# Kernel tuning notes

Measured on AMD Instinct MI355X. Metric: run time of the kernel, lower is better.

Reference implementation:

```python
import jax, jax.numpy as jnp
import numpy as np

B_, L_, H_ = 2, 2048, 2048          # batch, seq_len, hidden_size
I_, N_, NH, P_ = 4096, 128, 64, 64   # intermediate, ssm_state, num_heads, head_dim
K_, CH = 4, 256                      # conv kernel, chunk size
DT_MIN, DT_MAX = 0.0, 1e10


def setup_inputs() -> dict:
    key = jax.random.key(0)
    ks = jax.random.split(key, 8)
    conv_dim = I_ + 2 * N_
    proj_out = 2 * (I_ + N_) + NH
    return {
        "hidden_states": jax.random.normal(ks[0], (B_, L_, H_), jnp.float32),
        "W_in": jax.random.normal(ks[1], (proj_out, H_), jnp.float32) * 0.02,
        "conv_w": jax.random.normal(ks[2], (conv_dim, 1, K_), jnp.float32) * 0.2,
        "conv_b": jnp.zeros((conv_dim,), jnp.float32),
        "dt_bias": jax.random.uniform(ks[3], (NH,), jnp.float32),
        "A_log": jnp.log(jax.random.uniform(ks[4], (NH,), jnp.float32, 1.0, 16.0)),
        "D": jnp.ones((NH,), jnp.float32),
        "norm_w": jnp.ones((I_,), jnp.float32),
        "W_out": jax.random.normal(ks[5], (H_, I_), jnp.float32) * 0.02,
    }


def _segsum(x):
    # stable segment-sum: out[..., i, j] = sum_{k=j+1..i} x[..., k] for i>=j, else -inf
    T = x.shape[-1]
    xr = jnp.broadcast_to(x[..., None], x.shape + (T,))
    lower = jnp.tril(jnp.ones((T, T), bool), -1)
    s = jnp.cumsum(jnp.where(lower, xr, 0.0), axis=-2)
    return jnp.where(jnp.tril(jnp.ones((T, T), bool)), s, -jnp.inf)


def reference(hidden_states, W_in, conv_w, conv_b, dt_bias, A_log, D, norm_w, W_out):
    b, L, _ = hidden_states.shape
    proj = hidden_states @ W_in.T                       # (b, L, 2*(I+N)+H)
    z, xBC, dt = jnp.split(proj, [I_, 2 * I_ + 2 * N_], axis=-1)

    # depthwise causal conv1d + silu
    x_t = xBC.transpose(0, 2, 1)                        # (b, conv_dim, L)
    conv = jax.lax.conv_general_dilated(
        x_t, conv_w, (1,), [(K_ - 1, 0)],
        dimension_numbers=("NCH", "OIH", "NCH"), feature_group_count=I_ + 2 * N_)
    xBC = jax.nn.silu((conv + conv_b[None, :, None]).transpose(0, 2, 1))
    x, Bm, Cm = jnp.split(xBC, [I_, I_ + N_], axis=-1)  # (b,L,I) (b,L,N) (b,L,N)

    # ---- SSD naive (chunked state-space-duality scan) ----
    A = -jnp.exp(A_log.astype(jnp.float32))             # (h,)
    dt = jnp.clip(jax.nn.softplus(dt + dt_bias), DT_MIN, DT_MAX)  # (b,L,h)
    x4 = x.reshape(b, L, NH, P_)
    pad = (-L) % CH
    padf = lambda t: jnp.pad(t, [(0, 0), (0, pad)] + [(0, 0)] * (t.ndim - 2))
    D_res = D[None, None, :, None] * padf(x4)           # (b, Lp, h, p)
    xs = padf(x4 * dt[..., None])
    Ah = padf(A[None, None, :] * dt)                    # (b, Lp, h)
    Bc, Cc = padf(Bm), padf(Cm)
    c = (L + pad) // CH
    xs = xs.reshape(b, c, CH, NH, P_)                   # (b,c,l,h,p)
    Ah = Ah.reshape(b, c, CH, NH).transpose(0, 3, 1, 2) # (b,h,c,l)
    Bc = Bc.reshape(b, c, CH, N_)
    Cc = Cc.reshape(b, c, CH, N_)

    A_cs = jnp.cumsum(Ah, axis=-1)                      # (b,h,c,l)
    Lm = jnp.exp(_segsum(Ah))                           # (b,h,c,l,l)
    # intra-chunk (diagonal block) output; B/C shared across heads (n_groups=1)
    Y_diag = jnp.einsum("bcln,bcsn,bhcls,bcshp->bclhp", Cc, Bc, Lm, xs)

    decay_states = jnp.exp(A_cs[..., -1:] - A_cs)       # (b,h,c,l)
    states = jnp.einsum("bcln,bhcl,bclhp->bchpn", Bc, decay_states, xs)
    states = jnp.concatenate([jnp.zeros_like(states[:, :1]), states], axis=1)
    decay_chunk = jnp.exp(_segsum(jnp.pad(A_cs[..., -1], [(0, 0), (0, 0), (1, 0)])))
    new_states = jnp.einsum("bhzc,bchpn->bzhpn", decay_chunk, states)
    states = new_states[:, :-1]                         # (b,c,h,p,n)
    Y_off = jnp.einsum("bcln,bchpn,bhcl->bclhp", Cc, states, jnp.exp(A_cs))

    y = (Y_diag + Y_off).reshape(b, c * CH, NH, P_) + D_res
    y = y[:, :L].reshape(b, L, I_)

    # gated RMSNorm (normalize=True: multiply by silu(residual) before norm)
    yf = y.astype(jnp.float32) * jax.nn.silu(z.astype(jnp.float32))
    yf = yf * jax.lax.rsqrt(jnp.mean(yf * yf, -1, keepdims=True) + 1e-5) * norm_w
    return yf.astype(hidden_states.dtype) @ W_out.T
```

## Files before the change

kernel.cpp:

```cpp
#include <hip/hip_runtime.h>
#include <hip/hip_bf16.h>
#include <math.h>


#define B_SZ 2
#define L_SZ 2048
#define H_SZ 2048
#define I_SZ 4096
#define N_SZ 128
#define NH_SZ 64
#define P_SZ 64
#define CH_SZ 256
#define NC_SZ 8
#define PROJ_SZ 8512
#define CONV_SZ 4352
#define XOFF 4096
#define DTOFF 8448
#define BOFF 4096
#define COFF 4224

typedef __attribute__((ext_vector_type(8))) short short8_t;
typedef __attribute__((ext_vector_type(4))) float float4_t;

#define GLDS(gp, lp)                                                   \
  __builtin_amdgcn_global_load_lds(                                    \
      (const __attribute__((address_space(1))) void*)(gp),             \
      (__attribute__((address_space(3))) void*)(lp), 16, 0, 0)

__device__ __forceinline__ float bf2f(unsigned short u) {
  union { unsigned int i; float f; } v; v.i = ((unsigned int)u) << 16; return v.f;
}
__device__ __forceinline__ unsigned short f2bf(float f) {
  union { float f; unsigned int i; } v; v.f = f;
  unsigned int b = v.i + 0x7fffu + ((v.i >> 16) & 1u);
  return (unsigned short)(b >> 16);
}
__device__ __forceinline__ void unpack8(uint4 v, float* f) {
  f[0] = bf2f((unsigned short)(v.x & 0xffffu)); f[1] = bf2f((unsigned short)(v.x >> 16));
  f[2] = bf2f((unsigned short)(v.y & 0xffffu)); f[3] = bf2f((unsigned short)(v.y >> 16));
  f[4] = bf2f((unsigned short)(v.z & 0xffffu)); f[5] = bf2f((unsigned short)(v.z >> 16));
  f[6] = bf2f((unsigned short)(v.w & 0xffffu)); f[7] = bf2f((unsigned short)(v.w >> 16));
}
__device__ __forceinline__ float silu_f(float x) { return x / (1.f + expf(-x)); }

__device__ __forceinline__ float load1(const void* p, long long e, int fp32) {
  return fp32 ? ((const float*)p)[e] : bf2f(((const unsigned short*)p)[e]);
}
__device__ __forceinline__ void load4(const void* p, long long e, int fp32, float* f) {
  if (fp32) {
    float4 a = *(const float4*)((const float*)p + e);
    f[0] = a.x; f[1] = a.y; f[2] = a.z; f[3] = a.w;
  } else {
    uint2 v = *(const uint2*)((const unsigned short*)p + e);
    f[0] = bf2f((unsigned short)(v.x & 0xffffu)); f[1] = bf2f((unsigned short)(v.x >> 16));
    f[2] = bf2f((unsigned short)(v.y & 0xffffu)); f[3] = bf2f((unsigned short)(v.y >> 16));
  }
}
__device__ __forceinline__ void load8(const void* p, long long e, int fp32, float* f) {
  if (fp32) {
    float4 a = *(const float4*)((const float*)p + e);
    float4 b = *(const float4*)((const float*)p + e + 4);
    f[0] = a.x; f[1] = a.y; f[2] = a.z; f[3] = a.w;
    f[4] = b.x; f[5] = b.y; f[6] = b.z; f[7] = b.w;
  } else {
    uint4 v = *(const uint4*)((const unsigned short*)p + e);
    unpack8(v, f);
  }
}

__global__ void detect_k(const void* p0, const void* p1, const void* p2,
                         const void* p3, const void* p4, const void* p5,
                         const void* p6, const void* p7, const void* p8,
                         int n0, int n1, int n2, int n3, int n4, int n5,
                         int n6, int n7, int n8, int* flags) {
  __shared__ int pe, po;
  const void* ps[9] = {p0, p1, p2, p3, p4, p5, p6, p7, p8};
  int ns[9] = {n0, n1, n2, n3, n4, n5, n6, n7, n8};
  int t = threadIdx.x;
  for (int i = 0; i < 9; i++) {
    if (t == 0) { pe = 0; po = 0; }
    __syncthreads();
    int S = ns[i] < 256 ? ns[i] : 256;
    if (t < S) {
      unsigned short u = ((const unsigned short*)ps[i])[t];
      int ex = (u >> 7) & 0xFF;
      int plaus = ((u & 0x7FFFu) != 0) && (ex >= 0x70) && (ex <= 0x8F);
      if (plaus) { if (t & 1) atomicAdd(&po, 1); else atomicAdd(&pe, 1); }
    }
    __syncthreads();
    if (t == 0) flags[i] = (2 * pe < po) ? 1 : 0;
    __syncthreads();
  }
  if (t == 0) { flags[14] = 0; flags[15] = 0; }
}

__global__ __launch_bounds__(256)
void cvt_bf16_k(const void* __restrict__ src, unsigned short* __restrict__ dst,
                long long n8, const int* __restrict__ flags, int fi) {
  long long g = (long long)blockIdx.x * 256 + threadIdx.x;
  if (g >= n8) return;
  long long e = g * 8;
  if (flags[fi]) {
    const float* s = (const float*)src + e;
    float4 a = *(const float4*)s;
    float4 b = *(const float4*)(s + 4);
    unsigned short o[8] = {f2bf(a.x), f2bf(a.y), f2bf(a.z), f2bf(a.w),
                           f2bf(b.x), f2bf(b.y), f2bf(b.z), f2bf(b.w)};
    *(uint4*)(dst + e) = *(const uint4*)o;
  } else {
    *(uint4*)(dst + e) = *(const uint4*)((const unsigned short*)src + e);
  }
}

template <int OUT_MODE>
__global__ __launch_bounds__(256)
void gemm_dma_k(const unsigned short* __restrict__ A,
                const unsigned short* __restrict__ B,
                void* __restrict__ Cptr, int M, int N, int K,
                int lda, int ldb, int ldc,
                const int* __restrict__ flags, int fo) {
  __shared__ unsigned short As[128 * 32];
  __shared__ unsigned short Bs[128 * 32];
  const int t = threadIdx.x;
  const int lane = t & 63;
  const int wave = t >> 6;
  const int quad = lane >> 4;
  const int l16 = lane & 15;
  const int m0 = blockIdx.y * 128, n0 = blockIdx.x * 128;
  const int wm = (wave >> 1) * 64, wn = (wave & 1) * 64;
  const int ofp = (OUT_MODE == 2) ? flags[fo] : 0;

  float4_t acc[4][4];
#pragma unroll
  for (int i = 0; i < 4; i++)
#pragma unroll
    for (int j = 0; j < 4; j++) acc[i][j] = (float4_t){0.f, 0.f, 0.f, 0.f};

  const int rr = lane >> 2;
  const int ks = (lane & 3) * 8;
  const long long aR0 = (long long)(m0 + wave * 16 + rr) * lda + ks;
  const long long aR1 = aR0 + (long long)64 * lda;
  const long long bR0 = (long long)(n0 + wave * 16 + rr) * ldb + ks;
  const long long bR1 = bR0 + (long long)64 * ldb;
  unsigned short* asd0 = &As[(wave * 16) * 32];
  unsigned short* asd1 = &As[(64 + wave * 16) * 32];
  unsigned short* bsd0 = &Bs[(wave * 16) * 32];
  unsigned short* bsd1 = &Bs[(64 + wave * 16) * 32];

  for (int k0 = 0; k0 < K; k0 += 32) {
    __syncthreads();
    GLDS(A + aR0 + k0, asd0);
    GLDS(A + aR1 + k0, asd1);
    GLDS(B + bR0 + k0, bsd0);
    GLDS(B + bR1 + k0, bsd1);
    __syncthreads();
    short8_t afr[4], bfr[4];
#pragma unroll
    for (int i = 0; i < 4; i++)
      afr[i] = *(const short8_t*)&As[(wm + i * 16 + l16) * 32 + quad * 8];
#pragma unroll
    for (int j = 0; j < 4; j++)
      bfr[j] = *(const short8_t*)&Bs[(wn + j * 16 + l16) * 32 + quad * 8];
#pragma unroll
    for (int i = 0; i < 4; i++)
#pragma unroll
      for (int j = 0; j < 4; j++)
        acc[i][j] = __builtin_amdgcn_mfma_f32_16x16x32_bf16(
            afr[i], bfr[j], acc[i][j], 0, 0, 0);
  }
#pragma unroll
  for (int i = 0; i < 4; i++) {
#pragma unroll
    for (int r = 0; r < 4; r++) {
      const int m = m0 + wm + i * 16 + quad * 4 + r;
      const long long base = (long long)m * ldc;
#pragma unroll
      for (int j = 0; j < 4; j++) {
        const int n = n0 + wn + j * 16 + l16;
        if (n < N) {
          float v = acc[i][j][r];
          if (ofp) ((float*)Cptr)[base + n] = v;
          else     ((unsigned short*)Cptr)[base + n] = f2bf(v);
        }
      }
    }
  }
}

template <int OUT_MODE>
__global__ __launch_bounds__(256)
void gemm_bt_k(const void* __restrict__ A, const void* __restrict__ B,
               void* __restrict__ Cptr, int M, int N, int K,
               int lda, int ldb, int ldc,
               long long sA, long long sB, long long sC,
               const int* __restrict__ flags, int fa, int fb, int fo) {
  __shared__ float As[128][20];
  __shared__ float Bs[128][20];
  const int t = threadIdx.x;
  const int tx = t & 15, ty = t >> 4;
  const int m0 = blockIdx.y * 128, n0 = blockIdx.x * 128;
  const int afp = flags[fa], bfp = flags[fb];
  const int ofp = (OUT_MODE == 2) ? flags[fo] : (OUT_MODE == 1);
  const long long zoff = (long long)blockIdx.z;
  float* Cf = (float*)Cptr + zoff * sC;
  unsigned short* Cb = (unsigned short*)Cptr + zoff * sC;

  float acc[8][8];
#pragma unroll
  for (int i = 0; i < 8; i++)
#pragma unroll
    for (int j = 0; j < 8; j++) acc[i][j] = 0.f;

  const int rowS = t >> 1;
  const int kof  = (t & 1) * 8;
  const long long aRow = zoff * sA + (long long)(m0 + rowS) * lda + kof;
  const long long bRow = zoff * sB + (long long)(n0 + rowS) * ldb + kof;
  const bool bOK = (n0 + rowS) < N;

  for (int k0 = 0; k0 < K; k0 += 16) {
    float af[8], bf[8];
    load8(A, aRow + k0, afp, af);
    if (bOK) load8(B, bRow + k0, bfp, bf);
    else { bf[0]=bf[1]=bf[2]=bf[3]=bf[4]=bf[5]=bf[6]=bf[7]=0.f; }
    __syncthreads();
    *(float4*)&As[rowS][kof]     = make_float4(af[0], af[1], af[2], af[3]);
    *(float4*)&As[rowS][kof + 4] = make_float4(af[4], af[5], af[6], af[7]);
    *(float4*)&Bs[rowS][kof]     = make_float4(bf[0], bf[1], bf[2], bf[3]);
    *(float4*)&Bs[rowS][kof + 4] = make_float4(bf[4], bf[5], bf[6], bf[7]);
    __syncthreads();
#pragma unroll
    for (int kk = 0; kk < 16; kk += 2) {
      float2 a2[8], b2[8];
#pragma unroll
      for (int i = 0; i < 8; i++) a2[i] = *(const float2*)&As[ty + 16 * i][kk];
#pragma unroll
      for (int j = 0; j < 8; j++) b2[j] = *(const float2*)&Bs[tx + 16 * j][kk];
#pragma unroll
      for (int i = 0; i < 8; i++)
#pragma unroll
        for (int j = 0; j < 8; j++) {
          acc[i][j] = fmaf(a2[i].x, b2[j].x, acc[i][j]);
          acc[i][j] = fmaf(a2[i].y, b2[j].y, acc[i][j]);
        }
    }
  }
#pragma unroll
  for (int i = 0; i < 8; i++) {
    const int m = m0 + ty + 16 * i;
    const long long base = (long long)m * ldc;
#pragma unroll
    for (int j = 0; j < 8; j++) {
      const int n = n0 + tx + 16 * j;
      if (n < N) {
        if (ofp) Cf[base + n] = acc[i][j];
        else     Cb[base + n] = f2bf(acc[i][j]);
      }
    }
  }
}

__global__ __launch_bounds__(256)
void conv_silu_k(const unsigned short* __restrict__ proj,
                 const void* __restrict__ cw,
                 const void* __restrict__ cb,
                 unsigned short* __restrict__ convx,
                 const int* __restrict__ flags) {
  const int total = B_SZ * L_SZ * (CONV_SZ / 4);
  int g = blockIdx.x * 256 + threadIdx.x;
  if (g >= total) return;
  const int fw = flags[2], fb = flags[3];
  int c4 = g % (CONV_SZ / 4);
  int bl = g / (CONV_SZ / 4);
  int l = bl & (L_SZ - 1);
  int ch = c4 * 4;
  float w0[8], w1[8];
  load8(cw, (long long)ch * 4, fw, w0);
  load8(cw, (long long)ch * 4 + 8, fw, w1);
  float accv[4];
  load4(cb, ch, fb, accv);
  float acc0 = accv[0], acc1 = accv[1], acc2 = accv[2], acc3 = accv[3];
  const long long rb = (long long)(bl - l);
#pragma unroll
  for (int k = 0; k < 4; k++) {
    int ls = l - 3 + k;
    if (ls < 0) continue;
    uint2 xv = *(const uint2*)(proj + (rb + ls) * PROJ_SZ + XOFF + ch);
    float x0 = bf2f((unsigned short)(xv.x & 0xffffu));
    float x1 = bf2f((unsigned short)(xv.x >> 16));
    float x2 = bf2f((unsigned short)(xv.y & 0xffffu));
    float x3 = bf2f((unsigned short)(xv.y >> 16));
    acc0 = fmaf(x0, w0[k], acc0);
    acc1 = fmaf(x1, w0[4 + k], acc1);
    acc2 = fmaf(x2, w1[k], acc2);
    acc3 = fmaf(x3, w1[4 + k], acc3);
  }
  unsigned short o0 = f2bf(silu_f(acc0));
  unsigned short o1 = f2bf(silu_f(acc1));
  unsigned short o2 = f2bf(silu_f(acc2));
  unsigned short o3 = f2bf(silu_f(acc3));
  *(uint2*)(convx + (long long)bl * CONV_SZ + ch) =
      make_uint2((unsigned int)o0 | ((unsigned int)o1 << 16),
                 (unsigned int)o2 | ((unsigned int)o3 << 16));
}

__global__ __launch_bounds__(256)
void dt_prep_k(const unsigned short* __restrict__ proj,
               const void* __restrict__ dt_bias,
               float* __restrict__ dtv, const int* __restrict__ flags) {
  int g = blockIdx.x * 256 + threadIdx.x;
  int h = g & 63;
  long long bl = g >> 6;
  float v = bf2f(proj[bl * PROJ_SZ + DTOFF + h]) + load1(dt_bias, h, flags[4]);
  float sp = (v > 20.f) ? v : log1pf(expf(v));
  dtv[g] = sp;
}

__global__ __launch_bounds__(256)
void acs_scan_k(const float* __restrict__ dtv,
                const void* __restrict__ A_log,
                float* __restrict__ acs, const int* __restrict__ flags) {
  __shared__ float sd[256];
  int blk = blockIdx.x;
  int h = blk & 63;
  int bc = blk >> 6;
  int l = threadIdx.x;
  float Ah = -expf(load1(A_log, h, flags[5]));
  long long row = (long long)bc * CH_SZ + l;
  sd[l] = Ah * dtv[row * NH_SZ + h];
  for (int off = 1; off < 256; off <<= 1) {
    __syncthreads();
    float tv = (l >= off) ? sd[l - off] : 0.f;
    __syncthreads();
    sd[l] += tv;
  }
  acs[(long long)blk * CH_SZ + l] = sd[l];
}

__global__ __launch_bounds__(256)
void chunk_states_k(const unsigned short* __restrict__ convx,
                    const float* __restrict__ dtv,
                    const float* __restrict__ acs,
                    float* __restrict__ stc) {
  __shared__ float Bw[32][128];
  __shared__ float xw[32][64];
  int blk = blockIdx.x;
  int h = blk & 63;
  int bc = blk >> 6;
  int t = threadIdx.x;
  const int p0 = (t & 15) * 4, n0 = (t >> 4) * 8;
  const float* acsb = acs + (long long)blk * 256;
  const float alast = acsb[255];
  float acc[4][8];
#pragma unroll
  for (int i = 0; i < 4; i++)
#pragma unroll
    for (int j = 0; j < 8; j++) acc[i][j] = 0.f;
  const long long row0 = (long long)bc * 256;

  for (int lt0 = 0; lt0 < 256; lt0 += 32) {
    __syncthreads();
#pragma unroll
    for (int q = 0; q < 4; q++) {
      int idx4 = (t + 256 * q) * 4;
      int r = idx4 >> 7, n = idx4 & 127;
      uint2 v = *(const uint2*)(convx + (row0 + lt0 + r) * CONV_SZ + BOFF + n);
      Bw[r][n]     = bf2f((unsigned short)(v.x & 0xffffu));
      Bw[r][n + 1] = bf2f((unsigned short)(v.x >> 16));
      Bw[r][n + 2] = bf2f((unsigned short)(v.y & 0xffffu));
      Bw[r][n + 3] = bf2f((unsigned short)(v.y >> 16));
    }
#pragma unroll
    for (int q = 0; q < 2; q++) {
      int idx4 = (t + 256 * q) * 4;
      int r = idx4 >> 6, p = idx4 & 63;
      long long lg = row0 + lt0 + r;
      float sc = dtv[lg * NH_SZ + h] * expf(alast - acsb[lt0 + r]);
      uint2 v = *(const uint2*)(convx + lg * CONV_SZ + h * 64 + p);
      xw[r][p]     = bf2f((unsigned short)(v.x & 0xffffu)) * sc;
      xw[r][p + 1] = bf2f((unsigned short)(v.x >> 16)) * sc;
      xw[r][p + 2] = bf2f((unsigned short)(v.y & 0xffffu)) * sc;
      xw[r][p + 3] = bf2f((unsigned short)(v.y >> 16)) * sc;
    }
    __syncthreads();
#pragma unroll 4
    for (int lt = 0; lt < 32; lt++) {
      float4 xv = *(const float4*)&xw[lt][p0];
      float4 b0 = *(const float4*)&Bw[lt][n0];
      float4 b1 = *(const float4*)&Bw[lt][n0 + 4];
      float xa[4] = {xv.x, xv.y, xv.z, xv.w};
      float ba[8] = {b0.x, b0.y, b0.z, b0.w, b1.x, b1.y, b1.z, b1.w};
#pragma unroll
      for (int i = 0; i < 4; i++)
#pragma unroll
        for (int j = 0; j < 8; j++) acc[i][j] = fmaf(xa[i], ba[j], acc[i][j]);
    }
  }
  float* outb = stc + (long long)blk * 8192;
#pragma unroll
  for (int i = 0; i < 4; i++) {
    *(float4*)&outb[(p0 + i) * 128 + n0] =
        make_float4(acc[i][0], acc[i][1], acc[i][2], acc[i][3]);
    *(float4*)&outb[(p0 + i) * 128 + n0 + 4] =
        make_float4(acc[i][4], acc[i][5], acc[i][6], acc[i][7]);
  }
}

__global__ __launch_bounds__(256)
void recur_k(float* __restrict__ stc, const float* __restrict__ acs) {
  int blk = blockIdx.x;
  int b = blk >> 6, h = blk & 63;
  int t = threadIdx.x;
  float S[32];
#pragma unroll
  for (int j = 0; j < 32; j++) S[j] = 0.f;
  for (int z = 0; z < 8; z++) {
    long long bz = ((long long)b * 8 + z) * 64 + h;
    long long base = bz * 8192;
    float e = expf(acs[bz * 256 + 255]);
#pragma unroll
    for (int j = 0; j < 32; j++) {
      int idx = j * 256 + t;
      float cs = stc[base + idx];
      stc[base + idx] = S[j];
      S[j] = fmaf(e, S[j], cs);
    }
  }
}

__global__ __launch_bounds__(256)
void yoff_k(const unsigned short* __restrict__ convx,
            const float* __restrict__ sti,
            const float* __restrict__ acs,
            const void* __restrict__ Dw,
            float* __restrict__ y, const int* __restrict__ flags) {
  __shared__ float SIt[128][68];
  __shared__ unsigned short Ct[64][128];
  int blk = blockIdx.x;
  int h = blk & 63;
  int bc = blk >> 6;
  int t = threadIdx.x;
  const int txp = t & 15, lq = t >> 4;
  const float Dh = load1(Dw, h, flags[6]);
  const float* sib = sti + (long long)blk * 8192;
#pragma unroll 4
  for (int q = 0; q < 32; q++) {
    int idx = t + 256 * q;
    SIt[idx & 127][idx >> 7] = sib[idx];
  }
  const float* acsb = acs + (long long)blk * 256;
  const long long row0 = (long long)bc * 256;
  for (int ltile = 0; ltile < 4; ltile++) {
    __syncthreads();
#pragma unroll 4
    for (int q = 0; q < 32; q++) {
      int idx = t + 256 * q;
      int lr = idx >> 7, n = idx & 127;
      Ct[lr][n] = convx[(row0 + ltile * 64 + lr) * CONV_SZ + COFF + n];
    }
    __syncthreads();
    float acc[4][4] = {};
#pragma unroll 4
    for (int n = 0; n < 128; n++) {
      float4 sv = *(const float4*)&SIt[n][txp * 4];
      float c0 = bf2f(Ct[lq * 4 + 0][n]);
      float c1 = bf2f(Ct[lq * 4 + 1][n]);
      float c2 = bf2f(Ct[lq * 4 + 2][n]);
      float c3 = bf2f(Ct[lq * 4 + 3][n]);
      acc[0][0] = fmaf(c0, sv.x, acc[0][0]); acc[0][1] = fmaf(c0, sv.y, acc[0][1]);
      acc[0][2] = fmaf(c0, sv.z, acc[0][2]); acc[0][3] = fmaf(c0, sv.w, acc[0][3]);
      acc[1][0] = fmaf(c1, sv.x, acc[1][0]); acc[1][1] = fmaf(c1, sv.y, acc[1][1]);
      acc[1][2] = fmaf(c1, sv.z, acc[1][2]); acc[1][3] = fmaf(c1, sv.w, acc[1][3]);
      acc[2][0] = fmaf(c2, sv.x, acc[2][0]); acc[2][1] = fmaf(c2, sv.y, acc[2][1]);
      acc[2][2] = fmaf(c2, sv.z, acc[2][2]); acc[2][3] = fmaf(c2, sv.w, acc[2][3]);
      acc[3][0] = fmaf(c3, sv.x, acc[3][0]); acc[3][1] = fmaf(c3, sv.y, acc[3][1]);
      acc[3][2] = fmaf(c3, sv.z, acc[3][2]); acc[3][3] = fmaf(c3, sv.w, acc[3][3]);
    }
#pragma unroll
    for (int i = 0; i < 4; i++) {
      int lloc = ltile * 64 + lq * 4 + i;
      long long row = row0 + lloc;
      float ex = expf(acsb[lloc]);
      uint2 xv = *(const uint2*)(convx + row * CONV_SZ + h * 64 + txp * 4);
      float4 o;
      o.x = fmaf(ex, acc[i][0], Dh * bf2f((unsigned short)(xv.x & 0xffffu)));
      o.y = fmaf(ex, acc[i][1], Dh * bf2f((unsigned short)(xv.x >> 16)));
      o.z = fmaf(ex, acc[i][2], Dh * bf2f((unsigned short)(xv.y & 0xffffu)));
      o.w = fmaf(ex, acc[i][3], Dh * bf2f((unsigned short)(xv.y >> 16)));
      *(float4*)&y[row * I_SZ + h * 64 + txp * 4] = o;
    }
  }
}

__global__ __launch_bounds__(256)
void ydiag_k(const unsigned short* __restrict__ convx,
             const float* __restrict__ dtv,
             const float* __restrict__ acs,
             const float* __restrict__ Gmat,
             float* __restrict__ y) {
  __shared__ float acs_s[256];
  __shared__ float xsT[64][68];
  __shared__ float Mt[64][66];
  int blk = blockIdx.x;
  int h = blk & 63;
  int bc = blk >> 6;
  int t = threadIdx.x;
  const int txp = t & 15, lq = t >> 4;
  acs_s[t] = acs[(long long)blk * 256 + t];
  const long long row0 = (long long)bc * 256;
  const float* Gb = Gmat + (long long)bc * 65536;
  for (int ltile = 0; ltile < 4; ltile++) {
    float acc[4][4] = {};
    for (int stile = 0; stile <= ltile; stile++) {
      __syncthreads();
#pragma unroll 4
      for (int q = 0; q < 16; q++) {
        int idx = t + 256 * q;
        int ss = idx >> 6, p = idx & 63;
        long long row = row0 + stile * 64 + ss;
        xsT[ss][p] = bf2f(convx[row * CONV_SZ + h * 64 + p]) * dtv[row * NH_SZ + h];
      }
#pragma unroll 4
      for (int q = 0; q < 16; q++) {
        int idx = t + 256 * q;
        int lr = idx >> 6, ss = idx & 63;
        int lg = ltile * 64 + lr, sg = stile * 64 + ss;
        float m = 0.f;
        if (sg <= lg) m = Gb[(long long)lg * 256 + sg] * expf(acs_s[lg] - acs_s[sg]);
        Mt[lr][ss] = m;
      }
      __syncthreads();
#pragma unroll 4
      for (int ss = 0; ss < 64; ss++) {
        float4 xv = *(const float4*)&xsT[ss][txp * 4];
        float m0 = Mt[lq * 4 + 0][ss];
        float m1 = Mt[lq * 4 + 1][ss];
        float m2 = Mt[lq * 4 + 2][ss];
        float m3 = Mt[lq * 4 + 3][ss];
        acc[0][0] = fmaf(m0, xv.x, acc[0][0]); acc[0][1] = fmaf(m0, xv.y, acc[0][1]);
        acc[0][2] = fmaf(m0, xv.z, acc[0][2]); acc[0][3] = fmaf(m0, xv.w, acc[0][3]);
        acc[1][0] = fmaf(m1, xv.x, acc[1][0]); acc[1][1] = fmaf(m1, xv.y, acc[1][1]);
        acc[1][2] = fmaf(m1, xv.z, acc[1][2]); acc[1][3] = fmaf(m1, xv.w, acc[1][3]);
        acc[2][0] = fmaf(m2, xv.x, acc[2][0]); acc[2][1] = fmaf(m2, xv.y, acc[2][1]);
        acc[2][2] = fmaf(m2, xv.z, acc[2][2]); acc[2][3] = fmaf(m2, xv.w, acc[2][3]);
        acc[3][0] = fmaf(m3, xv.x, acc[3][0]); acc[3][1] = fmaf(m3, xv.y, acc[3][1]);
        acc[3][2] = fmaf(m3, xv.z, acc[3][2]); acc[3][3] = fmaf(m3, xv.w, acc[3][3]);
      }
    }
#pragma unroll
    for (int i = 0; i < 4; i++) {
      long long row = row0 + ltile * 64 + lq * 4 + i;
      float* yp = &y[row * I_SZ + h * 64 + txp * 4];
      float4 cur = *(float4*)yp;
      cur.x += acc[i][0]; cur.y += acc[i][1]; cur.z += acc[i][2]; cur.w += acc[i][3];
      *(float4*)yp = cur;
    }
  }
}

__global__ __launch_bounds__(256)
void norm_k(const float* __restrict__ y,
            const unsigned short* __restrict__ proj,
            const void* __restrict__ nw,
            unsigned short* __restrict__ yfb, const int* __restrict__ flags) {
  __shared__ float red[4];
  __shared__ float sc_s;
  int row = blockIdx.x;
  int t = threadIdx.x;
  const int fn = flags[7];
  const float* yr = y + (long long)row * I_SZ;
  const unsigned short* zr = proj + (long long)row * PROJ_SZ;
  float g[16];
  float ss = 0.f;
#pragma unroll
  for (int q = 0; q < 4; q++) {
    int i0 = q * 1024 + t * 4;
    float4 yv = *(const float4*)&yr[i0];
    uint2 zv = *(const uint2*)&zr[i0];
    float z0 = bf2f((unsigned short)(zv.x & 0xffffu));
    float z1 = bf2f((unsigned short)(zv.x >> 16));
    float z2 = bf2f((unsigned short)(zv.y & 0xffffu));
    float z3 = bf2f((unsigned short)(zv.y >> 16));
    float g0 = yv.x * silu_f(z0), g1 = yv.y * silu_f(z1);
    float g2 = yv.z * silu_f(z2), g3 = yv.w * silu_f(z3);
    g[q * 4 + 0] = g0; g[q * 4 + 1] = g1; g[q * 4 + 2] = g2; g[q * 4 + 3] = g3;
    ss += g0 * g0 + g1 * g1 + g2 * g2 + g3 * g3;
  }
#pragma unroll
  for (int off = 32; off > 0; off >>= 1) ss += __shfl_down(ss, off, 64);
  if ((t & 63) == 0) red[t >> 6] = ss;
  __syncthreads();
  if (t == 0) sc_s = rsqrtf((red[0] + red[1] + red[2] + red[3]) * (1.f / 4096.f) + 1e-5f);
  __syncthreads();
  float sc = sc_s;
#pragma unroll
  for (int q = 0; q < 4; q++) {
    int i0 = q * 1024 + t * 4;
    float nv[4];
    load4(nw, i0, fn, nv);
    unsigned short o0 = f2bf(g[q * 4 + 0] * sc * nv[0]);
    unsigned short o1 = f2bf(g[q * 4 + 1] * sc * nv[1]);
    unsigned short o2 = f2bf(g[q * 4 + 2] * sc * nv[2]);
    unsigned short o3 = f2bf(g[q * 4 + 3] * sc * nv[3]);
    *(uint2*)&yfb[(long long)row * I_SZ + i0] =
        make_uint2((unsigned int)o0 | ((unsigned int)o1 << 16),
                   (unsigned int)o2 | ((unsigned int)o3 << 16));
  }
}

extern "C" void kernel_launch(void* const* d_in, const int* in_sizes, int n_in,
                              void* d_out, int out_size, void* d_ws, size_t ws_size,
                              hipStream_t stream) {
  const void* hs     = d_in[0];
  const void* W_in   = d_in[1];
  const void* conv_w = d_in[2];
  const void* conv_b = d_in[3];
  const void* dt_b   = d_in[4];
  const void* A_log  = d_in[5];
  const void* Dw     = d_in[6];
  const void* nw     = d_in[7];
  const void* W_out  = d_in[8];

  char* ws = (char*)d_ws;
  size_t off = 0;
  auto alloc = [&](size_t bytes) -> void* {
    void* p = ws + off;
    off += (bytes + 255) & ~(size_t)255;
    return p;
  };
  const long long ML = (long long)B_SZ * L_SZ;
  int* flags = (int*)alloc(64);
  unsigned short* proj  = (unsigned short*)alloc(ML * PROJ_SZ * 2);
  unsigned short* convx = (unsigned short*)alloc(ML * CONV_SZ * 2);
  float* dtv  = (float*)alloc(ML * NH_SZ * 4);
  float* acsb = (float*)alloc((long long)B_SZ * NC_SZ * NH_SZ * CH_SZ * 4);
  float* Gm   = (float*)alloc((long long)B_SZ * NC_SZ * CH_SZ * CH_SZ * 4);
  float* stc  = (float*)alloc((long long)B_SZ * NC_SZ * NH_SZ * P_SZ * N_SZ * 4);
  float* yb   = (float*)alloc(ML * I_SZ * 4);
  unsigned short* yfb = (unsigned short*)stc;
  unsigned short* hs_bf   = (unsigned short*)yb;
  unsigned short* Win_bf  = (unsigned short*)yb + 8388608;
  unsigned short* Wout_bf = (unsigned short*)yb;
  (void)n_in; (void)out_size;
  if (off > ws_size) return;

  dim3 blk(256);
  detect_k<<<1, blk, 0, stream>>>(hs, W_in, conv_w, conv_b, dt_b, A_log, Dw, nw, W_out,
                                  in_sizes[0], in_sizes[1], in_sizes[2], in_sizes[3],
                                  in_sizes[4], in_sizes[5], in_sizes[6], in_sizes[7],
                                  in_sizes[8], flags);
  cvt_bf16_k<<<dim3(4096), blk, 0, stream>>>(hs, hs_bf, 1048576LL, flags, 0);
  cvt_bf16_k<<<dim3(8512), blk, 0, stream>>>(W_in, Win_bf, 2179072LL, flags, 1);
  gemm_dma_k<0><<<dim3(67, 32, 1), blk, 0, stream>>>(
      hs_bf, Win_bf, proj, 4096, PROJ_SZ, H_SZ, H_SZ, H_SZ, PROJ_SZ, flags, 15);
  conv_silu_k<<<dim3((B_SZ * L_SZ * (CONV_SZ / 4) + 255) / 256), blk, 0, stream>>>(
      proj, conv_w, conv_b, convx, flags);
  dt_prep_k<<<dim3((unsigned)(ML * NH_SZ / 256)), blk, 0, stream>>>(proj, dt_b, dtv, flags);
  acs_scan_k<<<dim3(B_SZ * NC_SZ * NH_SZ), blk, 0, stream>>>(dtv, A_log, acsb, flags);
  gemm_bt_k<1><<<dim3(2, 2, 16), blk, 0, stream>>>(
      (const unsigned short*)convx + COFF, (const unsigned short*)convx + BOFF,
      Gm, 256, 256, 128, CONV_SZ, CONV_SZ, 256,
      (long long)256 * CONV_SZ, (long long)256 * CONV_SZ, 65536,
      flags, 15, 15, 15);
  chunk_states_k<<<dim3(1024), blk, 0, stream>>>(convx, dtv, acsb, stc);
  recur_k<<<dim3(B_SZ * NH_SZ), blk, 0, stream>>>(stc, acsb);
  yoff_k<<<dim3(1024), blk, 0, stream>>>(convx, stc, acsb, Dw, yb, flags);
  ydiag_k<<<dim3(1024), blk, 0, stream>>>(convx, dtv, acsb, Gm, yb);
  norm_k<<<dim3((unsigned)ML), blk, 0, stream>>>(yb, proj, nw, yfb, flags);
  cvt_bf16_k<<<dim3(4096), blk, 0, stream>>>(W_out, Wout_bf, 1048576LL, flags, 8);
  gemm_dma_k<2><<<dim3(16, 32, 1), blk, 0, stream>>>(
      yfb, Wout_bf, d_out, 4096, H_SZ, I_SZ, I_SZ, I_SZ, H_SZ, flags, 0);
}
```

Baseline: 823.5 us.

## Add 256x256 eight-phase pipelined GEMM for input projection with tile swizzle

```diff
diff --git a/kernel.cpp b/kernel.cpp
--- a/kernel.cpp
+++ b/kernel.cpp
@@ -112,6 +112,163 @@
   }
 }
 
+#define MFMA_ACC(d, a, b) \
+  d = __builtin_amdgcn_mfma_f32_16x16x32_bf16(a, b, d, 0, 0, 0)
+#define LDA_FR(buf, i, kk) \
+  (*(const short8_t*)&As[(buf)*16384 + (wm*128 + (i)*16 + l16)*64 + \
+                         (((((kk)<<2) + quad) ^ l7) << 3)])
+#define LDB_FR(buf, j, kk) \
+  (*(const short8_t*)&Bs[(buf)*16384 + (wn*64 + (j)*16 + l16)*64 + \
+                         (((((kk)<<2) + quad) ^ l7) << 3)])
+#define STAGE_A(h, tile, buf) do {                                          \
+    GLDS(aSrc[h][0] + ((long long)(tile) << 6),                             \
+         &As[(buf)*16384 + (h)*8192 + (wave*16)*64]);                       \
+    GLDS(aSrc[h][1] + ((long long)(tile) << 6),                             \
+         &As[(buf)*16384 + (h)*8192 + (wave*16 + 8)*64]);                   \
+  } while (0)
+#define STAGE_B(h, tile, buf) do {                                          \
+    GLDS(bSrc[h][0] + ((long long)(tile) << 6),                             \
+         &Bs[(buf)*16384 + (h)*8192 + (wave*16)*64]);                       \
+    GLDS(bSrc[h][1] + ((long long)(tile) << 6),                             \
+         &Bs[(buf)*16384 + (h)*8192 + (wave*16 + 8)*64]);                   \
+  } while (0)
+
+__global__ __launch_bounds__(512, 2)
+void gemm_8ph_k(const unsigned short* __restrict__ A,
+                const unsigned short* __restrict__ B,
+                unsigned short* __restrict__ C,
+                int N, int K, int lda, int ldb, int ldc, int gxTiles) {
+  __shared__ alignas(16) unsigned short As[2 * 256 * 64];
+  __shared__ alignas(16) unsigned short Bs[2 * 256 * 64];
+  const int t = threadIdx.x;
+  const int lane = t & 63;
+  const int wave = t >> 6;
+  const int quad = lane >> 4;
+  const int l16 = lane & 15;
+  const int l7 = lane & 7;
+  const int l3 = lane >> 3;
+  const int wm = wave >> 2;
+  const int wn = wave & 3;
+
+  int id = blockIdx.x;
+  const int nwg = gridDim.x;
+  int swz = id;
+  if ((nwg & 7) == 0) swz = (id & 7) * (nwg >> 3) + (id >> 3);
+  const int band = gxTiles << 2;
+  const int by = (swz & 3) + ((swz / band) << 2);
+  const int bx = (swz >> 2) % gxTiles;
+  const int m0 = by << 8;
+  const int n0 = bx << 8;
+  const int NT = K >> 6;
+
+  const int kperm = ((l7 ^ l3) << 3);
+  const unsigned short* aSrc[2][2];
+  const unsigned short* bSrc[2][2];
+#pragma unroll
+  for (int h = 0; h < 2; ++h)
+#pragma unroll
+    for (int c = 0; c < 2; ++c) {
+      const int rloc = h * 128 + wave * 16 + c * 8 + l3;
+      aSrc[h][c] = A + (long long)(m0 + rloc) * lda + kperm;
+      int bn = n0 + rloc;
+      if (bn > N - 1) bn = N - 1;
+      bSrc[h][c] = B + (long long)bn * ldb + kperm;
+    }
+
+  float4_t acc[8][4];
+#pragma unroll
+  for (int i = 0; i < 8; ++i)
+#pragma unroll
+    for (int j = 0; j < 4; ++j) acc[i][j] = (float4_t){0.f, 0.f, 0.f, 0.f};
+
+  STAGE_A(0, 0, 0); STAGE_A(1, 0, 0);
+  STAGE_B(0, 0, 0); STAGE_B(1, 0, 0);
+  STAGE_B(0, 1, 1); STAGE_B(1, 1, 1);
+  asm volatile("s_waitcnt vmcnt(4)" ::: "memory");
+  __builtin_amdgcn_s_barrier();
+
+  short8_t af[4][2], bf[4][2];
+  for (int tt = 0; tt < NT; ++tt) {
+    const int rb = tt & 1, nb = rb ^ 1;
+#pragma unroll
+    for (int i = 0; i < 4; ++i) { af[i][0] = LDA_FR(rb, i, 0); af[i][1] = LDA_FR(rb, i, 1); }
+#pragma unroll
+    for (int j = 0; j < 2; ++j) { bf[j][0] = LDB_FR(rb, j, 0); bf[j][1] = LDB_FR(rb, j, 1); }
+    if (tt + 1 < NT) STAGE_A(0, tt + 1, nb);
+    asm volatile("s_waitcnt lgkmcnt(8)" ::: "memory");
+    __builtin_amdgcn_s_barrier();
+    asm volatile("s_waitcnt lgkmcnt(0)" ::: "memory");
+    __builtin_amdgcn_s_setprio(1);
+#pragma unroll
+    for (int i = 0; i < 4; ++i)
+#pragma unroll
+      for (int j = 0; j < 2; ++j) {
+        MFMA_ACC(acc[i][j], af[i][0], bf[j][0]);
+        MFMA_ACC(acc[i][j], af[i][1], bf[j][1]);
+      }
+    __builtin_amdgcn_s_setprio(0);
+    __builtin_amdgcn_s_barrier();
+#pragma unroll
+    for (int j = 2; j < 4; ++j) { bf[j][0] = LDB_FR(rb, j, 0); bf[j][1] = LDB_FR(rb, j, 1); }
+    if (tt + 1 < NT) STAGE_A(1, tt + 1, nb);
+    __builtin_amdgcn_s_barrier();
+    asm volatile("s_waitcnt lgkmcnt(0)" ::: "memory");
+    __builtin_amdgcn_s_setprio(1);
+#pragma unroll
+    for (int i = 0; i < 4; ++i)
+#pragma unroll
+      for (int j = 2; j < 4; ++j) {
+        MFMA_ACC(acc[i][j], af[i][0], bf[j][0]);
+        MFMA_ACC(acc[i][j], af[i][1], bf[j][1]);
+      }
+    __builtin_amdgcn_s_setprio(0);
+    __builtin_amdgcn_s_barrier();
+#pragma unroll
+    for (int i = 0; i < 4; ++i) { af[i][0] = LDA_FR(rb, 4 + i, 0); af[i][1] = LDA_FR(rb, 4 + i, 1); }
+    if (tt + 2 < NT) STAGE_B(0, tt + 2, rb);
+    __builtin_amdgcn_s_barrier();
+    asm volatile("s_waitcnt lgkmcnt(0)" ::: "memory");
+    __builtin_amdgcn_s_setprio(1);
+#pragma unroll
+    for (int i = 0; i < 4; ++i)
+#pragma unroll
+      for (int j = 0; j < 2; ++j) {
+        MFMA_ACC(acc[4 + i][j], af[i][0], bf[j][0]);
+        MFMA_ACC(acc[4 + i][j], af[i][1], bf[j][1]);
+      }
+    __builtin_amdgcn_s_setprio(0);
+    __builtin_amdgcn_s_barrier();
+    if (tt + 2 < NT) STAGE_B(1, tt + 2, rb);
+    __builtin_amdgcn_s_barrier();
+    __builtin_amdgcn_s_setprio(1);
+#pragma unroll
+    for (int i = 0; i < 4; ++i)
+#pragma unroll
+      for (int j = 2; j < 4; ++j) {
+        MFMA_ACC(acc[4 + i][j], af[i][0], bf[j][0]);
+        MFMA_ACC(acc[4 + i][j], af[i][1], bf[j][1]);
+      }
+    __builtin_amdgcn_s_setprio(0);
+    if (tt < NT - 2) asm volatile("s_waitcnt vmcnt(4)" ::: "memory");
+    else             asm volatile("s_waitcnt vmcnt(0)" ::: "memory");
+    __builtin_amdgcn_s_barrier();
+  }
+
+#pragma unroll
+  for (int i = 0; i < 8; ++i) {
+#pragma unroll
+    for (int r = 0; r < 4; ++r) {
+      const int m = m0 + wm * 128 + i * 16 + quad * 4 + r;
+      const long long cb = (long long)m * ldc;
+#pragma unroll
+      for (int j = 0; j < 4; ++j) {
+        const int n = n0 + wn * 64 + j * 16 + l16;
+        if (n < N) C[cb + n] = f2bf(acc[i][j][r]);
+      }
+    }
+  }
+}
+
 template <int OUT_MODE>
 __global__ __launch_bounds__(256)
 void gemm_dma_k(const unsigned short* __restrict__ A,
@@ -126,7 +283,17 @@
   const int wave = t >> 6;
   const int quad = lane >> 4;
   const int l16 = lane & 15;
-  const int m0 = blockIdx.y * 128, n0 = blockIdx.x * 128;
+  int bx = blockIdx.x, by = blockIdx.y;
+  {
+    const int nwg = gridDim.x * gridDim.y;
+    if ((nwg & 7) == 0 && (gridDim.y & 3) == 0) {
+      int id = blockIdx.y * gridDim.x + blockIdx.x;
+      int swz = (id & 7) * (nwg >> 3) + (id >> 3);
+      by = (swz & 3) + ((swz / (gridDim.x << 2)) << 2);
+      bx = (swz >> 2) % gridDim.x;
+    }
+  }
+  const int m0 = by * 128, n0 = bx * 128;
   const int wm = (wave >> 1) * 64, wn = (wave & 1) * 64;
   const int ofp = (OUT_MODE == 2) ? flags[fo] : 0;
 
@@ -650,8 +817,11 @@
                                   in_sizes[8], flags);
   cvt_bf16_k<<<dim3(4096), blk, 0, stream>>>(hs, hs_bf, 1048576LL, flags, 0);
   cvt_bf16_k<<<dim3(8512), blk, 0, stream>>>(W_in, Win_bf, 2179072LL, flags, 1);
-  gemm_dma_k<0><<<dim3(67, 32, 1), blk, 0, stream>>>(
-      hs_bf, Win_bf, proj, 4096, PROJ_SZ, H_SZ, H_SZ, H_SZ, PROJ_SZ, flags, 15);
+  gemm_8ph_k<<<dim3(512), dim3(512), 0, stream>>>(
+      hs_bf, Win_bf, proj, PROJ_SZ, H_SZ, H_SZ, H_SZ, PROJ_SZ, 32);
+  gemm_dma_k<0><<<dim3(3, 32), blk, 0, stream>>>(
+      hs_bf, Win_bf + 8192LL * 2048, proj + 8192, 4096, 320, H_SZ,
+      H_SZ, H_SZ, PROJ_SZ, flags, 15);
   conv_silu_k<<<dim3((B_SZ * L_SZ * (CONV_SZ / 4) + 255) / 256), blk, 0, stream>>>(
       proj, conv_w, conv_b, convx, flags);
   dt_prep_k<<<dim3((unsigned)(ML * NH_SZ / 256)), blk, 0, stream>>>(proj, dt_b, dtv, flags);
```

Result: faster. 796.5 us (-3.3%).

## Double-buffer bf16 GEMM with 64-wide K tiles, XOR LDS swizzle, and tile remap

Applied to the files above, without the earlier changes.

```diff
diff --git a/kernel.cpp b/kernel.cpp
--- a/kernel.cpp
+++ b/kernel.cpp
@@ -112,75 +112,119 @@
   }
 }
 
+#define MFMA_ACC(d, a, b) \
+  d = __builtin_amdgcn_mfma_f32_16x16x32_bf16(a, b, d, 0, 0, 0)
+#define LDA2(buf, i, kk) \
+  (*(const short8_t*)&As2[(buf)*8192 + (wm*64 + (i)*16 + l16)*64 + \
+                          (((((kk)<<2) + quad) ^ l7) << 3)])
+#define LDB2(buf, j, kk) \
+  (*(const short8_t*)&Bs2[(buf)*8192 + (wn*64 + (j)*16 + l16)*64 + \
+                          (((((kk)<<2) + quad) ^ l7) << 3)])
+
 template <int OUT_MODE>
-__global__ __launch_bounds__(256)
-void gemm_dma_k(const unsigned short* __restrict__ A,
+__global__ __launch_bounds__(256, 2)
+void gemm_2ph_k(const unsigned short* __restrict__ A,
                 const unsigned short* __restrict__ B,
-                void* __restrict__ Cptr, int M, int N, int K,
-                int lda, int ldb, int ldc,
+                void* __restrict__ Cptr,
+                int N, int K, int lda, int ldb, int ldc, int gxTiles,
                 const int* __restrict__ flags, int fo) {
-  __shared__ unsigned short As[128 * 32];
-  __shared__ unsigned short Bs[128 * 32];
+  __shared__ alignas(16) unsigned short As2[2 * 128 * 64];
+  __shared__ alignas(16) unsigned short Bs2[2 * 128 * 64];
   const int t = threadIdx.x;
   const int lane = t & 63;
   const int wave = t >> 6;
   const int quad = lane >> 4;
   const int l16 = lane & 15;
-  const int m0 = blockIdx.y * 128, n0 = blockIdx.x * 128;
-  const int wm = (wave >> 1) * 64, wn = (wave & 1) * 64;
+  const int l7 = lane & 7;
+  const int l3 = lane >> 3;
+  const int wm = wave >> 1;
+  const int wn = wave & 1;
   const int ofp = (OUT_MODE == 2) ? flags[fo] : 0;
 
+  int id = blockIdx.x;
+  const int nwg = gridDim.x;
+  int swz = id;
+  if ((nwg & 7) == 0) swz = (id & 7) * (nwg >> 3) + (id >> 3);
+  const int band = gxTiles << 2;
+  const int by = (swz & 3) + ((swz / band) << 2);
+  const int bx = (swz >> 2) % gxTiles;
+  const int m0 = by << 7;
+  const int n0 = bx << 7;
+  const int NT = K >> 6;
+
+  const int kperm = ((l7 ^ l3) << 3);
+  const unsigned short* aSrc[4];
+  const unsigned short* bSrc[4];
+#pragma unroll
+  for (int c = 0; c < 4; ++c) {
+    aSrc[c] = A + (long long)(m0 + wave * 32 + c * 8 + l3) * lda + kperm;
+    int bn = n0 + wave * 32 + c * 8 + l3;
+    if (bn > N - 1) bn = N - 1;
+    bSrc[c] = B + (long long)bn * ldb + kperm;
+  }
+
   float4_t acc[4][4];
 #pragma unroll
-  for (int i = 0; i < 4; i++)
-#pragma unroll
-    for (int j = 0; j < 4; j++) acc[i][j] = (float4_t){0.f, 0.f, 0.f, 0.f};
-
-  const int rr = lane >> 2;
-  const int ks = (lane & 3) * 8;
-  const long long aR0 = (long long)(m0 + wave * 16 + rr) * lda + ks;
-  const long long aR1 = aR0 + (long long)64 * lda;
-  const long long bR0 = (long long)(n0 + wave * 16 + rr) * ldb + ks;
-  const long long bR1 = bR0 + (long long)64 * ldb;
-  unsigned short* asd0 = &As[(wave * 16) * 32];
-  unsigned short* asd1 = &As[(64 + wave * 16) * 32];
-  unsigned short* bsd0 = &Bs[(wave * 16) * 32];
-  unsigned short* bsd1 = &Bs[(64 + wave * 16) * 32];
-
-  for (int k0 = 0; k0 < K; k0 += 32) {
-    __syncthreads();
-    GLDS(A + aR0 + k0, asd0);
-    GLDS(A + aR1 + k0, asd1);
-    GLDS(B + bR0 + k0, bsd0);
-    GLDS(B + bR1 + k0, bsd1);
-    __syncthreads();
-    short8_t afr[4], bfr[4];
-#pragma unroll
-    for (int i = 0; i < 4; i++)
-      afr[i] = *(const short8_t*)&As[(wm + i * 16 + l16) * 32 + quad * 8];
-#pragma unroll
-    for (int j = 0; j < 4; j++)
-      bfr[j] = *(const short8_t*)&Bs[(wn + j * 16 + l16) * 32 + quad * 8];
-#pragma unroll
-    for (int i = 0; i < 4; i++)
-#pragma unroll
-      for (int j = 0; j < 4; j++)
-        acc[i][j] = __builtin_amdgcn_mfma_f32_16x16x32_bf16(
-            afr[i], bfr[j], acc[i][j], 0, 0, 0);
-  }
-#pragma unroll
-  for (int i = 0; i < 4; i++) {
-#pragma unroll
-    for (int r = 0; r < 4; r++) {
-      const int m = m0 + wm + i * 16 + quad * 4 + r;
-      const long long base = (long long)m * ldc;
-#pragma unroll
-      for (int j = 0; j < 4; j++) {
-        const int n = n0 + wn + j * 16 + l16;
+  for (int i = 0; i < 4; ++i)
+#pragma unroll
+    for (int j = 0; j < 4; ++j) acc[i][j] = (float4_t){0.f, 0.f, 0.f, 0.f};
+
+#pragma unroll
+  for (int c = 0; c < 4; ++c) {
+    GLDS(aSrc[c], &As2[(wave * 32 + c * 8) * 64]);
+    GLDS(bSrc[c], &Bs2[(wave * 32 + c * 8) * 64]);
+  }
+  asm volatile("s_waitcnt vmcnt(0)" ::: "memory");
+  __builtin_amdgcn_s_barrier();
+
+  short8_t af[4], bfr[4];
+  for (int tt = 0; tt < NT; ++tt) {
+    const int rb = tt & 1, nb = rb ^ 1;
+#pragma unroll
+    for (int i = 0; i < 4; ++i) af[i] = LDA2(rb, i, 0);
+#pragma unroll
+    for (int j = 0; j < 4; ++j) bfr[j] = LDB2(rb, j, 0);
+    if (tt + 1 < NT) {
+      const long long ko = (long long)(tt + 1) << 6;
+#pragma unroll
+      for (int c = 0; c < 4; ++c) {
+        GLDS(aSrc[c] + ko, &As2[nb * 8192 + (wave * 32 + c * 8) * 64]);
+        GLDS(bSrc[c] + ko, &Bs2[nb * 8192 + (wave * 32 + c * 8) * 64]);
+      }
+    }
+    __builtin_amdgcn_s_setprio(1);
+#pragma unroll
+    for (int i = 0; i < 4; ++i)
+#pragma unroll
+      for (int j = 0; j < 4; ++j) MFMA_ACC(acc[i][j], af[i], bfr[j]);
+    __builtin_amdgcn_s_setprio(0);
+#pragma unroll
+    for (int i = 0; i < 4; ++i) af[i] = LDA2(rb, i, 1);
+#pragma unroll
+    for (int j = 0; j < 4; ++j) bfr[j] = LDB2(rb, j, 1);
+    __builtin_amdgcn_s_setprio(1);
+#pragma unroll
+    for (int i = 0; i < 4; ++i)
+#pragma unroll
+      for (int j = 0; j < 4; ++j) MFMA_ACC(acc[i][j], af[i], bfr[j]);
+    __builtin_amdgcn_s_setprio(0);
+    asm volatile("s_waitcnt vmcnt(0)" ::: "memory");
+    __builtin_amdgcn_s_barrier();
+  }
+
+#pragma unroll
+  for (int i = 0; i < 4; ++i) {
+#pragma unroll
+    for (int r = 0; r < 4; ++r) {
+      const int m = m0 + wm * 64 + i * 16 + quad * 4 + r;
+      const long long cb = (long long)m * ldc;
+#pragma unroll
+      for (int j = 0; j < 4; ++j) {
+        const int n = n0 + wn * 64 + j * 16 + l16;
         if (n < N) {
           float v = acc[i][j][r];
-          if (ofp) ((float*)Cptr)[base + n] = v;
-          else     ((unsigned short*)Cptr)[base + n] = f2bf(v);
+          if (ofp) ((float*)Cptr)[cb + n] = v;
+          else     ((unsigned short*)Cptr)[cb + n] = f2bf(v);
         }
       }
     }
@@ -650,8 +694,9 @@
                                   in_sizes[8], flags);
   cvt_bf16_k<<<dim3(4096), blk, 0, stream>>>(hs, hs_bf, 1048576LL, flags, 0);
   cvt_bf16_k<<<dim3(8512), blk, 0, stream>>>(W_in, Win_bf, 2179072LL, flags, 1);
-  gemm_dma_k<0><<<dim3(67, 32, 1), blk, 0, stream>>>(
-      hs_bf, Win_bf, proj, 4096, PROJ_SZ, H_SZ, H_SZ, H_SZ, PROJ_SZ, flags, 15);
+  gemm_2ph_k<0><<<dim3(2144), blk, 0, stream>>>(
+      hs_bf, Win_bf, proj, PROJ_SZ, H_SZ, H_SZ, H_SZ, PROJ_SZ, 67,
+      flags, 15);
   conv_silu_k<<<dim3((B_SZ * L_SZ * (CONV_SZ / 4) + 255) / 256), blk, 0, stream>>>(
       proj, conv_w, conv_b, convx, flags);
   dt_prep_k<<<dim3((unsigned)(ML * NH_SZ / 256)), blk, 0, stream>>>(proj, dt_b, dtv, flags);
@@ -667,6 +712,7 @@
   ydiag_k<<<dim3(1024), blk, 0, stream>>>(convx, dtv, acsb, Gm, yb);
   norm_k<<<dim3((unsigned)ML), blk, 0, stream>>>(yb, proj, nw, yfb, flags);
   cvt_bf16_k<<<dim3(4096), blk, 0, stream>>>(W_out, Wout_bf, 1048576LL, flags, 8);
-  gemm_dma_k<2><<<dim3(16, 32, 1), blk, 0, stream>>>(
-      yfb, Wout_bf, d_out, 4096, H_SZ, I_SZ, I_SZ, I_SZ, H_SZ, flags, 0);
-}
+  gemm_2ph_k<2><<<dim3(512), blk, 0, stream>>>(
+      yfb, Wout_bf, d_out, H_SZ, I_SZ, I_SZ, I_SZ, H_SZ, 16,
+      flags, 0);
+}
```

After: 732.9 us. -11.0%, faster.
